# Performance work log

Hardware: AMD Instinct MI355X
Metric: run time of the kernel (lower is better)

The kernel has to match this reference:

```python
import jax, jax.numpy as jnp
import numpy as np

N = 50000
E = 800000
NUM_GRAPHS = 128
X_IN, HID, EDGE_DIM = 64, 64, 16


def setup_inputs() -> dict:
    key = jax.random.key(0)
    ks = jax.random.split(key, 9)
    s = 0.05
    inp = {
        'x': jax.random.normal(ks[0], (N, X_IN), jnp.float32),
        'edge_index': jax.random.randint(ks[1], (2, E), 0, N, dtype=jnp.int32),
        'edge_attr': jax.random.normal(ks[2], (E, EDGE_DIM), jnp.float32),
        'batch': jnp.sort(jax.random.randint(ks[3], (N,), 0, NUM_GRAPHS, dtype=jnp.int32)),
        'w_fc1': jax.random.normal(ks[4], (EDGE_DIM, 1), jnp.float32) * s,
        'b_fc1': jnp.zeros((1,), jnp.float32),
    }
    dims = [(X_IN, HID), (HID, HID * 2), (HID * 2, HID)]
    for i, (din, dout) in enumerate(dims):
        k1, k2, k3 = jax.random.split(ks[5 + i], 3)
        inp[f'w1_{i}'] = jax.random.normal(k1, (din, dout), jnp.float32) * s
        inp[f'b1_{i}'] = jnp.zeros((dout,), jnp.float32)
        inp[f'w2_{i}'] = jax.random.normal(k2, (din, dout), jnp.float32) * s
        inp[f'w3_{i}'] = jax.random.normal(k3, (din, dout), jnp.float32) * s
        inp[f'b3_{i}'] = jnp.zeros((dout,), jnp.float32)
    return inp


def leconv(x, src, dst, ew, w1, b1, w2, w3, b3):
    # PyG LEConv: out_i = lin3(x_i) + sum_{j->i} e_ji * (lin1(x_j) - lin2(x_i))
    a = x @ w1 + b1          # lin1 (bias=True)   [N, out]
    b = x @ w2               # lin2 (bias=False)  [N, out]
    msg = ew[:, None] * (a[src] - b[dst])          # [E, out]
    agg = jax.ops.segment_sum(msg, dst, num_segments=N)
    return agg + x @ w3 + b3  # lin3 (bias=True)


def reference(x, edge_index, edge_attr, batch,
              w_fc1, b_fc1,
              w1_0, b1_0, w2_0, w3_0, b3_0,
              w1_1, b1_1, w2_1, w3_1, b3_1,
              w1_2, b1_2, w2_2, w3_2, b3_2):
    src, dst = edge_index[0], edge_index[1]
    ew = (edge_attr @ w_fc1 + b_fc1)[:, 0]         # fc1(edge_attr).squeeze(-1) -> [E]
    h = jax.nn.elu(leconv(x, src, dst, ew, w1_0, b1_0, w2_0, w3_0, b3_0))
    h = jax.nn.elu(leconv(h, src, dst, ew, w1_1, b1_1, w2_1, w3_1, b3_1))
    h = jax.nn.elu(leconv(h, src, dst, ew, w1_2, b1_2, w2_2, w3_2, b3_2))
    # global max pool over nodes of each graph -> [NUM_GRAPHS, HID]
    return jax.ops.segment_max(h, batch, num_segments=NUM_GRAPHS)
```

## Files before the change

kernel.cpp:

```cpp
#include <hip/hip_runtime.h>
#include <math.h>

#define N_NODES 50000
#define N_EDGES 800000
#define NUM_GRAPHS_ 128
#define SCAN_NB 98

typedef unsigned short u16;
typedef unsigned int u32;
typedef __attribute__((ext_vector_type(8))) short bf16x8;
typedef __attribute__((ext_vector_type(4))) float f32x4;

__device__ __forceinline__ float elu_f(float v) {
    return v > 0.f ? v : (__expf(v) - 1.f);
}
__device__ __forceinline__ u16 f2bf(float f) {
    u32 u = __float_as_uint(f);
    u += 0x7FFFu + ((u >> 16) & 1u);
    return (u16)(u >> 16);
}
__device__ __forceinline__ float bf2f(u16 h) {
    return __uint_as_float(((u32)h) << 16);
}
__device__ __forceinline__ void bfpair(u32 v, float& lo, float& hi) {
    lo = __uint_as_float(v << 16);
    hi = __uint_as_float(v & 0xFFFF0000u);
}
__device__ __forceinline__ u32 packbf(float lo, float hi) {
    return (u32)f2bf(lo) | ((u32)f2bf(hi) << 16);
}

__global__ void conv_x_kernel(const float* __restrict__ x, u16* __restrict__ xb,
                              int4* __restrict__ deg4) {
    int g = blockIdx.x * blockDim.x + threadIdx.x;
    if (g < N_NODES / 4) deg4[g] = (int4){0, 0, 0, 0};
    float4 v = ((const float4*)x)[g];
    uint2 o;
    o.x = packbf(v.x, v.y);
    o.y = packbf(v.z, v.w);
    ((uint2*)xb)[g] = o;
}

__global__ void ew_kernel(const float* __restrict__ edge_attr,
                          const float* __restrict__ w_fc1,
                          const float* __restrict__ b_fc1,
                          const int* __restrict__ edge_index,
                          float* __restrict__ ew,
                          int* __restrict__ deg) {
    int e = blockIdx.x * blockDim.x + threadIdx.x;
    if (e >= N_EDGES) return;
    const float4* ea = (const float4*)(edge_attr + (size_t)e * 16);
    const float4* wf = (const float4*)w_fc1;
    float acc = b_fc1[0];
#pragma unroll
    for (int i = 0; i < 4; i++) {
        float4 a = ea[i], w = wf[i];
        acc += a.x * w.x + a.y * w.y + a.z * w.z + a.w * w.w;
    }
    ew[e] = acc;
    atomicAdd(&deg[edge_index[N_EDGES + e]], 1);
}

__global__ __launch_bounds__(256) void scan1_kernel(const int* __restrict__ deg,
                                                    int* __restrict__ rowptr,
                                                    int* __restrict__ blk_sums) {
    __shared__ int sh[256];
    const int t = threadIdx.x;
    const int base = blockIdx.x * 512;
    const int i0 = base + 2 * t, i1 = i0 + 1;
    int d0 = 0, d1 = 0;
    if (i0 < N_NODES) d0 = deg[i0];
    if (i1 < N_NODES) d1 = deg[i1];
    const int pair = d0 + d1;
    int v = pair;
    sh[t] = v;
    __syncthreads();
#pragma unroll
    for (int off = 1; off < 256; off <<= 1) {
        int add = (t >= off) ? sh[t - off] : 0;
        __syncthreads();
        v += add;
        sh[t] = v;
        __syncthreads();
    }
    const int excl = v - pair;
    if (i0 < N_NODES) rowptr[i0] = excl;
    if (i1 < N_NODES) rowptr[i1] = excl + d0;
    if (t == 255) blk_sums[blockIdx.x] = v;
}

__global__ __launch_bounds__(128) void scan2_kernel(const int* __restrict__ blk_sums,
                                                    int* __restrict__ blk_offs,
                                                    int* __restrict__ rowptr) {
    __shared__ int sh[128];
    const int t = threadIdx.x;
    const int orig = (t < SCAN_NB) ? blk_sums[t] : 0;
    int v = orig;
    sh[t] = v;
    __syncthreads();
#pragma unroll
    for (int off = 1; off < 128; off <<= 1) {
        int add = (t >= off) ? sh[t - off] : 0;
        __syncthreads();
        v += add;
        sh[t] = v;
        __syncthreads();
    }
    if (t < SCAN_NB) blk_offs[t] = v - orig;
    if (t == 127) rowptr[N_NODES] = v;
}

__global__ void scan3_kernel(int* __restrict__ rowptr,
                             const int* __restrict__ blk_offs,
                             int* __restrict__ cur) {
    int i = blockIdx.x * blockDim.x + threadIdx.x;
    if (i >= N_NODES) return;
    const int v = rowptr[i] + blk_offs[i >> 9];
    rowptr[i] = v;
    cur[i] = v;
}

__global__ __launch_bounds__(256) void place_kernel(const int* __restrict__ edge_index,
                                                    const float* __restrict__ ew,
                                                    int* __restrict__ cur,
                                                    int2* __restrict__ csr) {
    const int e = blockIdx.x * 256 + threadIdx.x;
    if (e >= N_EDGES) return;
    const int d = edge_index[N_EDGES + e];
    const int slot = atomicAdd(&cur[d], 1);
    int2 ent;
    ent.x = edge_index[e];
    ent.y = __float_as_int(ew[e]);
    csr[slot] = ent;
}

template <int DIN, bool WRITE_C>
__global__ __launch_bounds__(256) void gather_kernel(
    const u16* __restrict__ xb, const int* __restrict__ rowptr,
    const int2* __restrict__ csr, u16* __restrict__ sb,
    u16* __restrict__ chb, float* __restrict__ c) {
    constexpr int CG = DIN / 4;
    constexpr int EG = 64 / CG;
    const int gid = blockIdx.x * 256 + threadIdx.x;
    const int node = gid >> 6;
    if (node >= N_NODES) return;
    const int lane = threadIdx.x & 63;
    const int cg = lane & (CG - 1);
    const int eg = lane / CG;
    const int beg = rowptr[node];
    const int end = rowptr[node + 1];
    const uint2* x2 = (const uint2*)xb;

    float a0 = 0.f, a1 = 0.f, a2 = 0.f, a3 = 0.f;
    float b0 = 0.f, b1 = 0.f, b2 = 0.f, b3 = 0.f;
    float wsum = 0.f;

    int p = beg + eg;
    for (; p + EG < end; p += 2 * EG) {
        int2 e0 = csr[p];
        int2 e1 = csr[p + EG];
        float w0 = __int_as_float(e0.y);
        float w1 = __int_as_float(e1.y);
        uint2 v0 = x2[(size_t)e0.x * CG + cg];
        uint2 v1 = x2[(size_t)e1.x * CG + cg];
        float f0, f1, f2, f3, g0, g1, g2, g3;
        bfpair(v0.x, f0, f1); bfpair(v0.y, f2, f3);
        bfpair(v1.x, g0, g1); bfpair(v1.y, g2, g3);
        a0 += w0 * f0; a1 += w0 * f1; a2 += w0 * f2; a3 += w0 * f3;
        b0 += w1 * g0; b1 += w1 * g1; b2 += w1 * g2; b3 += w1 * g3;
        wsum += w0 + w1;
    }
    if (p < end) {
        int2 e0 = csr[p];
        float w0 = __int_as_float(e0.y);
        uint2 v0 = x2[(size_t)e0.x * CG + cg];
        float f0, f1, f2, f3;
        bfpair(v0.x, f0, f1); bfpair(v0.y, f2, f3);
        a0 += w0 * f0; a1 += w0 * f1; a2 += w0 * f2; a3 += w0 * f3;
        wsum += w0;
    }
    a0 += b0; a1 += b1; a2 += b2; a3 += b3;

#pragma unroll
    for (int off = 32; off >= CG; off >>= 1) {
        a0 += __shfl_xor(a0, off);
        a1 += __shfl_xor(a1, off);
        a2 += __shfl_xor(a2, off);
        a3 += __shfl_xor(a3, off);
        wsum += __shfl_xor(wsum, off);
    }

    if (lane < CG) {
        uint2 so;
        so.x = packbf(a0, a1);
        so.y = packbf(a2, a3);
        ((uint2*)sb)[(size_t)node * CG + cg] = so;
        const float cn = WRITE_C ? wsum : c[node];
        uint2 hv = x2[(size_t)node * CG + cg];
        float h0, h1, h2, h3;
        bfpair(hv.x, h0, h1); bfpair(hv.y, h2, h3);
        uint2 co;
        co.x = packbf(cn * h0, cn * h1);
        co.y = packbf(cn * h2, cn * h3);
        ((uint2*)chb)[(size_t)node * CG + cg] = co;
    }
    if (WRITE_C && lane == 0) c[node] = wsum;
}

__global__ void pack_w_kernel(const float* __restrict__ w3_0, const float* __restrict__ w1_0, const float* __restrict__ w2_0,
                              const float* __restrict__ w3_1, const float* __restrict__ w1_1, const float* __restrict__ w2_1,
                              const float* __restrict__ w3_2, const float* __restrict__ w1_2, const float* __restrict__ w2_2,
                              u16* __restrict__ bp0, u16* __restrict__ bp1, u16* __restrict__ bp2) {
    int t = blockIdx.x * blockDim.x + threadIdx.x;
    if (t >= 7680) return;
    u16 buf[8];
    if (t < 4608) {
        int DIN, DOUT, lid;
        const float *w3, *w1, *w2;
        u16* bp;
        if (t < 1536) { DIN = 64; DOUT = 64;  lid = t;        w3 = w3_0; w1 = w1_0; w2 = w2_0; bp = bp0; }
        else          { DIN = 64; DOUT = 128; lid = t - 1536; w3 = w3_1; w1 = w1_1; w2 = w2_1; bp = bp1; }
        const int NT = DOUT / 16;
        const int lane = lid & 63;
        const int fragid = lid >> 6;
        const int chunk = fragid / NT;
        const int ntile = fragid % NT;
        const int n = ntile * 16 + (lane & 15);
        const int kbase = chunk * 32 + (lane >> 4) * 8;
#pragma unroll
        for (int j = 0; j < 8; j++) {
            int k = kbase + j;
            int region = k / DIN;
            int kk = k - region * DIN;
            float v = (region == 0) ? w3[kk * DOUT + n]
                    : (region == 1) ? w1[kk * DOUT + n]
                                    : -w2[kk * DOUT + n];
            buf[j] = f2bf(v);
        }
        *(bf16x8*)(bp + ((size_t)lid << 3)) = *(bf16x8*)buf;
    } else {
        const int lid = t - 4608;
        const int NT = 12;
        const int lane = lid & 63;
        const int fragid = lid >> 6;
        const int chunk = fragid / NT;
        const int ntile = fragid % NT;
        const int n = ntile * 16 + (lane & 15);
        const int kbase = chunk * 32 + (lane >> 4) * 8;
#pragma unroll
        for (int j = 0; j < 8; j++) {
            int k = kbase + j;
            float v = (n < 64)  ? w3_2[k * 64 + n]
                    : (n < 128) ? -w2_2[k * 64 + (n - 64)]
                                : w1_2[k * 64 + (n - 128)];
            buf[j] = f2bf(v);
        }
        *(bf16x8*)(bp2 + ((size_t)lid << 3)) = *(bf16x8*)buf;
    }
}

template <int DIN, int DOUT>
__global__ __launch_bounds__(256) void gemm_mfma(
    const u16* __restrict__ hb, const u16* __restrict__ sb,
    const u16* __restrict__ chb, const u16* __restrict__ Bp,
    const float* __restrict__ cvec, const float* __restrict__ bias1,
    const float* __restrict__ bias3, u16* __restrict__ outp) {
    constexpr int CH = DIN / 32;
    constexpr int CHUNKS = 3 * CH;
    constexpr int NT = DOUT / 16;
    const int tid = threadIdx.x;
    const int wv = tid >> 6;
    const int lane = tid & 63;
    const int l15 = lane & 15;
    const int q = lane >> 4;
    const int mhalf = wv & 1;
    const int nhalf = wv >> 1;
    const int row_base = blockIdx.x * 64 + mhalf * 32;
    const int nt0 = blockIdx.y * 4 + nhalf * 2;

    const int r0 = min(row_base + l15, N_NODES - 1);
    const int r1 = min(row_base + 16 + l15, N_NODES - 1);
    const int qo = q * 8;

    f32x4 acc00 = {0.f, 0.f, 0.f, 0.f};
    f32x4 acc01 = {0.f, 0.f, 0.f, 0.f};
    f32x4 acc10 = {0.f, 0.f, 0.f, 0.f};
    f32x4 acc11 = {0.f, 0.f, 0.f, 0.f};

#pragma unroll
    for (int chunk = 0; chunk < CHUNKS; chunk++) {
        const int region = chunk / CH;
        const int koff = (chunk - region * CH) * 32 + qo;
        const u16* A = (region == 0) ? hb : (region == 1) ? sb : chb;
        bf16x8 a0 = *(const bf16x8*)(A + (size_t)r0 * DIN + koff);
        bf16x8 a1 = *(const bf16x8*)(A + (size_t)r1 * DIN + koff);
        const u16* bp = Bp + (((size_t)(chunk * NT + nt0) * 64 + lane) << 3);
        bf16x8 bf0 = *(const bf16x8*)bp;
        bf16x8 bf1 = *(const bf16x8*)(bp + 64 * 8);
        acc00 = __builtin_amdgcn_mfma_f32_16x16x32_bf16(a0, bf0, acc00, 0, 0, 0);
        acc01 = __builtin_amdgcn_mfma_f32_16x16x32_bf16(a0, bf1, acc01, 0, 0, 0);
        acc10 = __builtin_amdgcn_mfma_f32_16x16x32_bf16(a1, bf0, acc10, 0, 0, 0);
        acc11 = __builtin_amdgcn_mfma_f32_16x16x32_bf16(a1, bf1, acc11, 0, 0, 0);
    }

#pragma unroll
    for (int ni = 0; ni < 2; ni++) {
        const int col = (nt0 + ni) * 16 + l15;
        const float B3 = bias3[col];
        const float B1 = bias1[col];
        const f32x4 am0 = ni ? acc01 : acc00;
        const f32x4 am1 = ni ? acc11 : acc10;
#pragma unroll
        for (int mi = 0; mi < 2; mi++) {
            const f32x4 av = mi ? am1 : am0;
#pragma unroll
            for (int reg = 0; reg < 4; reg++) {
                const int row = row_base + mi * 16 + q * 4 + reg;
                if (row < N_NODES) {
                    const float cv = cvec[row];
                    const float val = av[reg] + B3 + cv * B1;
                    outp[(size_t)row * DOUT + col] = f2bf(elu_f(val));
                }
            }
        }
    }
}

__global__ __launch_bounds__(256) void gemm_wide_kernel(
    const u16* __restrict__ hb, const u16* __restrict__ Bp,
    u16* __restrict__ zuy) {
    constexpr int NT = 12;
    const int tid = threadIdx.x;
    const int wv = tid >> 6;
    const int lane = tid & 63;
    const int l15 = lane & 15;
    const int q = lane >> 4;
    const int row_base = blockIdx.x * 64 + (wv & 1) * 32;
    const int nt0 = blockIdx.y * 4 + (wv >> 1) * 2;

    const int r0 = min(row_base + l15, N_NODES - 1);
    const int r1 = min(row_base + 16 + l15, N_NODES - 1);
    const int qo = q * 8;

    f32x4 acc00 = {0.f, 0.f, 0.f, 0.f};
    f32x4 acc01 = {0.f, 0.f, 0.f, 0.f};
    f32x4 acc10 = {0.f, 0.f, 0.f, 0.f};
    f32x4 acc11 = {0.f, 0.f, 0.f, 0.f};

#pragma unroll
    for (int chunk = 0; chunk < 4; chunk++) {
        const int koff = chunk * 32 + qo;
        bf16x8 a0 = *(const bf16x8*)(hb + (size_t)r0 * 128 + koff);
        bf16x8 a1 = *(const bf16x8*)(hb + (size_t)r1 * 128 + koff);
        const u16* bp = Bp + (((size_t)(chunk * NT + nt0) * 64 + lane) << 3);
        bf16x8 bf0 = *(const bf16x8*)bp;
        bf16x8 bf1 = *(const bf16x8*)(bp + 64 * 8);
        acc00 = __builtin_amdgcn_mfma_f32_16x16x32_bf16(a0, bf0, acc00, 0, 0, 0);
        acc01 = __builtin_amdgcn_mfma_f32_16x16x32_bf16(a0, bf1, acc01, 0, 0, 0);
        acc10 = __builtin_amdgcn_mfma_f32_16x16x32_bf16(a1, bf0, acc10, 0, 0, 0);
        acc11 = __builtin_amdgcn_mfma_f32_16x16x32_bf16(a1, bf1, acc11, 0, 0, 0);
    }

#pragma unroll
    for (int ni = 0; ni < 2; ni++) {
        const int col = (nt0 + ni) * 16 + l15;
        const f32x4 am0 = ni ? acc01 : acc00;
        const f32x4 am1 = ni ? acc11 : acc10;
#pragma unroll
        for (int mi = 0; mi < 2; mi++) {
            const f32x4 av = mi ? am1 : am0;
#pragma unroll
            for (int reg = 0; reg < 4; reg++) {
                const int row = row_base + mi * 16 + q * 4 + reg;
                if (row < N_NODES)
                    zuy[(size_t)row * 192 + col] = f2bf(av[reg]);
            }
        }
    }
}

__global__ __launch_bounds__(256) void gather2_kernel(
    const u16* __restrict__ zuy, const int* __restrict__ rowptr,
    const int2* __restrict__ csr, const float* __restrict__ c,
    const float* __restrict__ bias1, const float* __restrict__ bias3,
    u16* __restrict__ h3) {
    constexpr int CG = 16, EG = 4;
    const int gid = blockIdx.x * 256 + threadIdx.x;
    const int node = gid >> 6;
    if (node >= N_NODES) return;
    const int lane = threadIdx.x & 63;
    const int cg = lane & (CG - 1);
    const int eg = lane >> 4;
    const int beg = rowptr[node];
    const int end = rowptr[node + 1];

    float a0 = 0.f, a1 = 0.f, a2 = 0.f, a3 = 0.f;
    float b0 = 0.f, b1 = 0.f, b2 = 0.f, b3 = 0.f;

    int p = beg + eg;
    for (; p + EG < end; p += 2 * EG) {
        int2 e0 = csr[p];
        int2 e1 = csr[p + EG];
        float w0 = __int_as_float(e0.y);
        float w1 = __int_as_float(e1.y);
        uint2 v0 = ((const uint2*)(zuy + (size_t)e0.x * 192 + 128))[cg];
        uint2 v1 = ((const uint2*)(zuy + (size_t)e1.x * 192 + 128))[cg];
        float f0, f1, f2, f3, g0, g1, g2, g3;
        bfpair(v0.x, f0, f1); bfpair(v0.y, f2, f3);
        bfpair(v1.x, g0, g1); bfpair(v1.y, g2, g3);
        a0 += w0 * f0; a1 += w0 * f1; a2 += w0 * f2; a3 += w0 * f3;
        b0 += w1 * g0; b1 += w1 * g1; b2 += w1 * g2; b3 += w1 * g3;
    }
    if (p < end) {
        int2 e0 = csr[p];
        float w0 = __int_as_float(e0.y);
        uint2 v0 = ((const uint2*)(zuy + (size_t)e0.x * 192 + 128))[cg];
        float f0, f1, f2, f3;
        bfpair(v0.x, f0, f1); bfpair(v0.y, f2, f3);
        a0 += w0 * f0; a1 += w0 * f1; a2 += w0 * f2; a3 += w0 * f3;
    }
    a0 += b0; a1 += b1; a2 += b2; a3 += b3;

#pragma unroll
    for (int off = 32; off >= CG; off >>= 1) {
        a0 += __shfl_xor(a0, off);
        a1 += __shfl_xor(a1, off);
        a2 += __shfl_xor(a2, off);
        a3 += __shfl_xor(a3, off);
    }

    if (lane < CG) {
        const float cn = c[node];
        const u16* zr = zuy + (size_t)node * 192;
        uint2 zv = ((const uint2*)zr)[cg];
        uint2 uv = ((const uint2*)(zr + 64))[cg];
        float z0, z1, z2, z3, u0, u1, u2, u3;
        bfpair(zv.x, z0, z1); bfpair(zv.y, z2, z3);
        bfpair(uv.x, u0, u1); bfpair(uv.y, u2, u3);
        const float4 b3v = *(const float4*)(bias3 + cg * 4);
        const float4 b1v = *(const float4*)(bias1 + cg * 4);
        float o0 = elu_f(z0 + cn * u0 + a0 + b3v.x + cn * b1v.x);
        float o1 = elu_f(z1 + cn * u1 + a1 + b3v.y + cn * b1v.y);
        float o2 = elu_f(z2 + cn * u2 + a2 + b3v.z + cn * b1v.z);
        float o3 = elu_f(z3 + cn * u3 + a3 + b3v.w + cn * b1v.w);
        uint2 o;
        o.x = packbf(o0, o1);
        o.y = packbf(o2, o3);
        ((uint2*)h3)[(size_t)node * CG + cg] = o;
    }
}

__global__ void pool_kernel(const u16* __restrict__ h,
                            const int* __restrict__ batch,
                            float* __restrict__ out) {
    const int g = blockIdx.x;
    const int tid = threadIdx.x;
    int lo = 0, hi = N_NODES;
    while (lo < hi) { int mid = (lo + hi) >> 1; if (batch[mid] < g) lo = mid + 1; else hi = mid; }
    const int beg = lo;
    lo = beg; hi = N_NODES;
    while (lo < hi) { int mid = (lo + hi) >> 1; if (batch[mid] < g + 1) lo = mid + 1; else hi = mid; }
    const int end = lo;

    __shared__ float red[256];
    const int col = tid & 63;
    const int rg = tid >> 6;
    float m = -3.0e38f;
    for (int r = beg + rg; r < end; r += 4) m = fmaxf(m, bf2f(h[(size_t)r * 64 + col]));
    red[tid] = m;
    __syncthreads();
    if (tid < 64) {
        m = fmaxf(fmaxf(red[tid], red[tid + 64]), fmaxf(red[tid + 128], red[tid + 192]));
        out[g * 64 + tid] = m;
    }
}

extern "C" void kernel_launch(void* const* d_in, const int* in_sizes, int n_in,
                              void* d_out, int out_size, void* d_ws, size_t ws_size,
                              hipStream_t stream) {
    const float* x = (const float*)d_in[0];
    const int* ei = (const int*)d_in[1];
    const float* ea = (const float*)d_in[2];
    const int* batch = (const int*)d_in[3];
    const float* wfc = (const float*)d_in[4];
    const float* bfc = (const float*)d_in[5];
    const float* w1_0 = (const float*)d_in[6];
    const float* b1_0 = (const float*)d_in[7];
    const float* w2_0 = (const float*)d_in[8];
    const float* w3_0 = (const float*)d_in[9];
    const float* b3_0 = (const float*)d_in[10];
    const float* w1_1 = (const float*)d_in[11];
    const float* b1_1 = (const float*)d_in[12];
    const float* w2_1 = (const float*)d_in[13];
    const float* w3_1 = (const float*)d_in[14];
    const float* b3_1 = (const float*)d_in[15];
    const float* w1_2 = (const float*)d_in[16];
    const float* b1_2 = (const float*)d_in[17];
    const float* w2_2 = (const float*)d_in[18];
    const float* w3_2 = (const float*)d_in[19];
    const float* b3_2 = (const float*)d_in[20];
    float* out = (float*)d_out;

    char* ws = (char*)d_ws;
    float* ew      = (float*)(ws);
    float* c       = (float*)(ws + 3200000);
    int*   rowptr  = (int*)  (ws + 3800000);
    int2*  csr     = (int2*) (ws + 4000128);
    u16*   xb      = (u16*)  (ws + 10400128);
    u16*   sb      = (u16*)  (ws + 16800128);
    u16*   chb     = (u16*)  (ws + 29600128);
    u16*   h1      = (u16*)  (ws + 42400128);
    u16*   h2      = (u16*)  (ws + 48800128);
    u16*   h3      = (u16*)  (ws + 61600128);
    u16*   bp0     = (u16*)  (ws + 68000128);
    u16*   bp1     = (u16*)  (ws + 68024704);
    u16*   bp2     = (u16*)  (ws + 68073856);
    int*   deg     = (int*)  (ws + 68123008);
    int*   cur     = (int*)  (ws + 68323008);
    int* blk_sums  = (int*)  (ws + 68523008);
    int* blk_offs  = (int*)  (ws + 68523520);
    u16* zuy = sb;

    conv_x_kernel<<<3125, 256, 0, stream>>>(x, xb, (int4*)deg);
    ew_kernel<<<3125, 256, 0, stream>>>(ea, wfc, bfc, ei, ew, deg);
    pack_w_kernel<<<30, 256, 0, stream>>>(w3_0, w1_0, w2_0, w3_1, w1_1, w2_1,
                                          w3_2, w1_2, w2_2, bp0, bp1, bp2);
    scan1_kernel<<<SCAN_NB, 256, 0, stream>>>(deg, rowptr, blk_sums);
    scan2_kernel<<<1, 128, 0, stream>>>(blk_sums, blk_offs, rowptr);
    scan3_kernel<<<(N_NODES + 255) / 256, 256, 0, stream>>>(rowptr, blk_offs, cur);
    place_kernel<<<3125, 256, 0, stream>>>(ei, ew, cur, csr);

    const int RB = (N_NODES + 63) / 64;
    const int GBLK = (N_NODES * 64 + 255) / 256;

    gather_kernel<64, true><<<GBLK, 256, 0, stream>>>(xb, rowptr, csr, sb, chb, c);
    gemm_mfma<64, 64><<<dim3(RB, 1), 256, 0, stream>>>(xb, sb, chb, bp0, c, b1_0, b3_0, h1);

    gather_kernel<64, false><<<GBLK, 256, 0, stream>>>(h1, rowptr, csr, sb, chb, c);
    gemm_mfma<64, 128><<<dim3(RB, 2), 256, 0, stream>>>(h1, sb, chb, bp1, c, b1_1, b3_1, h2);

    gemm_wide_kernel<<<dim3(RB, 3), 256, 0, stream>>>(h2, bp2, zuy);
    gather2_kernel<<<GBLK, 256, 0, stream>>>(zuy, rowptr, csr, c, b1_2, b3_2, h3);

    pool_kernel<<<NUM_GRAPHS_, 256, 0, stream>>>(h3, batch, out);
}
```

Before: 374.5 us.

## Partition CSR placement by destination range using LDS atomics per block

The edge-weight kernel now writes packed (src, weight) COO entries plus a 16-bit destination array. The place kernel is rewritten so that each of 128 blocks owns a contiguous range of destination nodes. Each block scans every destination and claims slots through shared-memory atomic counters seeded from rowptr, rather than through contended global atomics on a separate cur array. This removes the cur buffer and the separate ew read, and h3 now reuses the xb buffer. The cost is that every block rereads the full 1.6 MB destination stream, and only 128 blocks run on the GPU.

Result: slower. 553.5 us (+47.8%).

```diff
diff --git a/kernel.cpp b/kernel.cpp
--- a/kernel.cpp
+++ b/kernel.cpp
@@ -5,6 +5,8 @@
 #define N_EDGES 800000
 #define NUM_GRAPHS_ 128
 #define SCAN_NB 98
+#define PL_BLOCKS 128
+#define PL_NODES 391
 
 typedef unsigned short u16;
 typedef unsigned int u32;
@@ -45,7 +47,8 @@
                           const float* __restrict__ w_fc1,
                           const float* __restrict__ b_fc1,
                           const int* __restrict__ edge_index,
-                          float* __restrict__ ew,
+                          int2* __restrict__ coo,
+                          u16* __restrict__ dst16,
                           int* __restrict__ deg) {
     int e = blockIdx.x * blockDim.x + threadIdx.x;
     if (e >= N_EDGES) return;
@@ -57,8 +60,13 @@
         float4 a = ea[i], w = wf[i];
         acc += a.x * w.x + a.y * w.y + a.z * w.z + a.w * w.w;
     }
-    ew[e] = acc;
-    atomicAdd(&deg[edge_index[N_EDGES + e]], 1);
+    int2 ent;
+    ent.x = edge_index[e];
+    ent.y = __float_as_int(acc);
+    coo[e] = ent;
+    const int d = edge_index[N_EDGES + e];
+    dst16[e] = (u16)d;
+    atomicAdd(&deg[d], 1);
 }
 
 __global__ __launch_bounds__(256) void scan1_kernel(const int* __restrict__ deg,
@@ -111,27 +119,36 @@
 }
 
 __global__ void scan3_kernel(int* __restrict__ rowptr,
-                             const int* __restrict__ blk_offs,
-                             int* __restrict__ cur) {
+                             const int* __restrict__ blk_offs) {
     int i = blockIdx.x * blockDim.x + threadIdx.x;
     if (i >= N_NODES) return;
-    const int v = rowptr[i] + blk_offs[i >> 9];
-    rowptr[i] = v;
-    cur[i] = v;
-}
-
-__global__ __launch_bounds__(256) void place_kernel(const int* __restrict__ edge_index,
-                                                    const float* __restrict__ ew,
-                                                    int* __restrict__ cur,
+    rowptr[i] += blk_offs[i >> 9];
+}
+
+__global__ __launch_bounds__(512) void place_kernel(const u16* __restrict__ dst16,
+                                                    const int2* __restrict__ coo,
+                                                    const int* __restrict__ rowptr,
                                                     int2* __restrict__ csr) {
-    const int e = blockIdx.x * 256 + threadIdx.x;
-    if (e >= N_EDGES) return;
-    const int d = edge_index[N_EDGES + e];
-    const int slot = atomicAdd(&cur[d], 1);
-    int2 ent;
-    ent.x = edge_index[e];
-    ent.y = __float_as_int(ew[e]);
-    csr[slot] = ent;
+    __shared__ int lcur[PL_NODES];
+    const int base = blockIdx.x * PL_NODES;
+    const int nloc = min(PL_NODES, N_NODES - base);
+    for (int i = threadIdx.x; i < nloc; i += 512) lcur[i] = rowptr[base + i];
+    __syncthreads();
+    const uint4* d8 = (const uint4*)dst16;
+    for (int chunk = threadIdx.x; chunk < N_EDGES / 8; chunk += 512) {
+        const uint4 v = d8[chunk];
+        const int e0 = chunk * 8;
+        const u32 w[4] = {v.x, v.y, v.z, v.w};
+#pragma unroll
+        for (int j = 0; j < 8; j++) {
+            const int d = (int)((j & 1) ? (w[j >> 1] >> 16) : (w[j >> 1] & 0xFFFFu));
+            const int dl = d - base;
+            if ((unsigned)dl < (unsigned)nloc) {
+                const int slot = atomicAdd(&lcur[dl], 1);
+                csr[slot] = coo[e0 + j];
+            }
+        }
+    }
 }
 
 template <int DIN, bool WRITE_C>
@@ -502,33 +519,33 @@
     float* out = (float*)d_out;
 
     char* ws = (char*)d_ws;
-    float* ew      = (float*)(ws);
-    float* c       = (float*)(ws + 3200000);
-    int*   rowptr  = (int*)  (ws + 3800000);
-    int2*  csr     = (int2*) (ws + 4000128);
-    u16*   xb      = (u16*)  (ws + 10400128);
-    u16*   sb      = (u16*)  (ws + 16800128);
-    u16*   chb     = (u16*)  (ws + 29600128);
-    u16*   h1      = (u16*)  (ws + 42400128);
-    u16*   h2      = (u16*)  (ws + 48800128);
-    u16*   h3      = (u16*)  (ws + 61600128);
-    u16*   bp0     = (u16*)  (ws + 68000128);
-    u16*   bp1     = (u16*)  (ws + 68024704);
-    u16*   bp2     = (u16*)  (ws + 68073856);
-    int*   deg     = (int*)  (ws + 68123008);
-    int*   cur     = (int*)  (ws + 68323008);
-    int* blk_sums  = (int*)  (ws + 68523008);
-    int* blk_offs  = (int*)  (ws + 68523520);
+    int2*  coo     = (int2*) (ws);
+    u16*   dst16   = (u16*)  (ws + 6400000);
+    float* c       = (float*)(ws + 8000000);
+    int*   rowptr  = (int*)  (ws + 8200000);
+    int2*  csr     = (int2*) (ws + 8400128);
+    u16*   xb      = (u16*)  (ws + 14800128);
+    u16*   sb      = (u16*)  (ws + 21200128);
+    u16*   chb     = (u16*)  (ws + 34000128);
+    u16*   h1      = (u16*)  (ws + 46800128);
+    u16*   h2      = (u16*)  (ws + 53200128);
+    u16*   bp0     = (u16*)  (ws + 66000128);
+    u16*   bp1     = (u16*)  (ws + 66024704);
+    u16*   bp2     = (u16*)  (ws + 66073856);
+    int*   deg     = (int*)  (ws + 66123008);
+    int* blk_sums  = (int*)  (ws + 66323008);
+    int* blk_offs  = (int*)  (ws + 66323520);
     u16* zuy = sb;
+    u16* h3  = xb;
 
     conv_x_kernel<<<3125, 256, 0, stream>>>(x, xb, (int4*)deg);
-    ew_kernel<<<3125, 256, 0, stream>>>(ea, wfc, bfc, ei, ew, deg);
+    ew_kernel<<<3125, 256, 0, stream>>>(ea, wfc, bfc, ei, coo, dst16, deg);
     pack_w_kernel<<<30, 256, 0, stream>>>(w3_0, w1_0, w2_0, w3_1, w1_1, w2_1,
                                           w3_2, w1_2, w2_2, bp0, bp1, bp2);
     scan1_kernel<<<SCAN_NB, 256, 0, stream>>>(deg, rowptr, blk_sums);
     scan2_kernel<<<1, 128, 0, stream>>>(blk_sums, blk_offs, rowptr);
-    scan3_kernel<<<(N_NODES + 255) / 256, 256, 0, stream>>>(rowptr, blk_offs, cur);
-    place_kernel<<<3125, 256, 0, stream>>>(ei, ew, cur, csr);
+    scan3_kernel<<<(N_NODES + 255) / 256, 256, 0, stream>>>(rowptr, blk_offs);
+    place_kernel<<<PL_BLOCKS, 512, 0, stream>>>(dst16, coo, rowptr, csr);
 
     const int RB = (N_NODES + 63) / 64;
     const int GBLK = (N_NODES * 64 + 255) / 256;
```
